# Kernel optimization log

Measured on AMD Instinct MI355X. Metric: run time of the kernel, lower is better.

Reference implementation:

```python
import jax, jax.numpy as jnp
import numpy as np

D_MODEL = 768
NUM_HEADS = 12
SEGMENT_LENGTHS = (2048, 4096, 8192)
DILATION_RATES = (1, 2, 4)
LN_EPS = 1e-5


def setup_inputs() -> dict:
    key = jax.random.key(0)
    ks = jax.random.split(key, 8)
    b, n, dm = 2, 8192, D_MODEL
    s = 1.0 / np.sqrt(dm)
    return {
        "x": jax.random.normal(ks[0], (b, n, dm), dtype=jnp.float32),
        "w_in": jax.random.normal(ks[1], (dm, dm), dtype=jnp.float32) * s,
        "b_in": jnp.zeros((dm,), dtype=jnp.float32),
        "w_out": jax.random.normal(ks[2], (dm, dm), dtype=jnp.float32) * s,
        "b_out": jnp.zeros((dm,), dtype=jnp.float32),
        "ln_gamma": jnp.ones((dm,), dtype=jnp.float32),
        "ln_beta": jnp.zeros((dm,), dtype=jnp.float32),
    }


def _dilated_attention(q, k, v):
    # q, k, v: (b, n, h, d)
    b, n, h, d = q.shape
    num_groups = len(DILATION_RATES)
    group_sizes = [h // num_groups] * num_groups
    for i in range(h % num_groups):
        group_sizes[i] += 1
    scale = 1.0 / jnp.sqrt(jnp.asarray(d, q.dtype))
    out = jnp.zeros_like(q)
    for i, (g, r, s) in enumerate(zip(group_sizes, DILATION_RATES, SEGMENT_LENGTHS)):
        offset = i % r
        hmin, hmax = i * g, (i + 1) * g
        nseg = n // s
        def slc(t):
            # (b, nseg, s, h, d) -> strided dilation slice + head group slice
            return t.reshape(b, nseg, s, h, d)[:, :, offset::r, hmin:hmax, :]
        qs, ks_, vs = slc(q), slc(k), slc(v)  # (b, nseg, se, g, d), se = s // r
        attn = jnp.einsum('bnqhd,bnkhd->bnhqk', qs, ks_) * scale
        attn = jax.nn.softmax(attn, axis=-1)
        x = jnp.einsum('bnhqk,bnkhd->bnqhd', attn, vs)  # (b, nseg, se, g, d)
        # renormalize by sum over (segment, within-segment) dims, as in source
        x = x / x.sum(axis=(1, 2), keepdims=True)
        out = (out.reshape(b, nseg, s, h, d)
                  .at[:, :, offset::r, hmin:hmax, :].add(x)
                  .reshape(b, n, h, d))
    return out / num_groups


def reference(x, w_in, b_in, w_out, b_out, ln_gamma, ln_beta):
    b, n, dm = x.shape
    hd = dm // NUM_HEADS
    # QKVProjectionOption.SAME: q = k = v = proj(x)
    q = x @ w_in.T + b_in
    qh = q.reshape(b, n, NUM_HEADS, hd)
    o = _dilated_attention(qh, qh, qh)
    o = o.reshape(b, n, dm)
    mu = o.mean(axis=-1, keepdims=True)
    var = ((o - mu) ** 2).mean(axis=-1, keepdims=True)
    o = (o - mu) / jnp.sqrt(var + LN_EPS) * ln_gamma + ln_beta
    return o @ w_out.T + b_out
```

## Files before the change

### kernel.cpp

```cpp
#include <hip/hip_runtime.h>
#include <hip/hip_bf16.h>
#include <math.h>

#define B_   2
#define N_   8192
#define DM   768
#define NH   12
#define HD   64

#define QL_ELEM_OFF 12582912ull
#define AC_OFF      12582912ull
#define SUMS_OFF    19922944ull

typedef short bf16x8 __attribute__((ext_vector_type(8)));
typedef _Float16 f16x8 __attribute__((ext_vector_type(8)));
typedef _Float16 f16x4 __attribute__((ext_vector_type(4)));
typedef float f32x4  __attribute__((ext_vector_type(4)));

__device__ __forceinline__ size_t ac_base(int grp) {
    return 8388608ull - (8388608ull >> grp);
}

__device__ __forceinline__ unsigned short f2bf(float f) {
    __hip_bfloat16 h = __float2bfloat16(f);
    return __builtin_bit_cast(unsigned short, h);
}
__device__ __forceinline__ float bf2f(unsigned short u) {
    __hip_bfloat16 h = __builtin_bit_cast(__hip_bfloat16, u);
    return __bfloat162float(h);
}
__device__ __forceinline__ void split2h(float f, _Float16& h, _Float16& l) {
    h = (_Float16)f;
    l = (_Float16)(f - (float)h);
}

#define SW(row, col) ((((row) << 6)) + ((((col) >> 3) ^ ((row) & 7)) << 3) + ((col) & 7))

__global__ __launch_bounds__(256) void gemm_mfma_split(
    const float* __restrict__ A, const float* __restrict__ W,
    const float* __restrict__ bias, float* __restrict__ C,
    _Float16* __restrict__ Ch, _Float16* __restrict__ Cl) {
    __shared__ unsigned short AsH[128][40];
    __shared__ unsigned short AsL[128][40];
    __shared__ unsigned short WsH[128][40];
    __shared__ unsigned short WsL[128][40];

    const int t    = threadIdx.x;
    const int lane = t & 63;
    const int wv   = t >> 6;
    const int c    = lane & 15, q = lane >> 4;
    const int mw   = (wv & 1) * 64, nw = (wv >> 1) * 64;
    const int m0   = blockIdx.x * 128, n0 = blockIdx.y * 128;

    const int srow = t >> 1;
    const int scol = (t & 1) * 16;
    const float* ap = A + (size_t)(m0 + srow) * DM + scol;
    const float* wp = W + (size_t)(n0 + srow) * DM + scol;

    f32x4 acc[4][4];
#pragma unroll
    for (int mi = 0; mi < 4; ++mi)
#pragma unroll
        for (int ni = 0; ni < 4; ++ni) {
            acc[mi][ni][0] = 0.f; acc[mi][ni][1] = 0.f;
            acc[mi][ni][2] = 0.f; acc[mi][ni][3] = 0.f;
        }

    for (int k0 = 0; k0 < DM; k0 += 32) {
        float av[16], wvv[16];
        *(float4*)&av[0]  = *(const float4*)(ap + k0);
        *(float4*)&av[4]  = *(const float4*)(ap + k0 + 4);
        *(float4*)&av[8]  = *(const float4*)(ap + k0 + 8);
        *(float4*)&av[12] = *(const float4*)(ap + k0 + 12);
        *(float4*)&wvv[0]  = *(const float4*)(wp + k0);
        *(float4*)&wvv[4]  = *(const float4*)(wp + k0 + 4);
        *(float4*)&wvv[8]  = *(const float4*)(wp + k0 + 8);
        *(float4*)&wvv[12] = *(const float4*)(wp + k0 + 12);
        __syncthreads();
#pragma unroll
        for (int i = 0; i < 16; ++i) {
            const float x = av[i];
            const unsigned short xh = f2bf(x);
            AsH[srow][scol + i] = xh;
            AsL[srow][scol + i] = f2bf(x - bf2f(xh));
            const float y = wvv[i];
            const unsigned short yh = f2bf(y);
            WsH[srow][scol + i] = yh;
            WsL[srow][scol + i] = f2bf(y - bf2f(yh));
        }
        __syncthreads();

        bf16x8 ah[4], al[4], bh[4], bl[4];
#pragma unroll
        for (int i = 0; i < 4; ++i) {
            ah[i] = *(const bf16x8*)&AsH[mw + i*16 + c][q*8];
            al[i] = *(const bf16x8*)&AsL[mw + i*16 + c][q*8];
            bh[i] = *(const bf16x8*)&WsH[nw + i*16 + c][q*8];
            bl[i] = *(const bf16x8*)&WsL[nw + i*16 + c][q*8];
        }
#pragma unroll
        for (int mi = 0; mi < 4; ++mi)
#pragma unroll
            for (int ni = 0; ni < 4; ++ni) {
                f32x4 v = acc[mi][ni];
                v = __builtin_amdgcn_mfma_f32_16x16x32_bf16(ah[mi], bl[ni], v, 0, 0, 0);
                v = __builtin_amdgcn_mfma_f32_16x16x32_bf16(al[mi], bh[ni], v, 0, 0, 0);
                v = __builtin_amdgcn_mfma_f32_16x16x32_bf16(ah[mi], bh[ni], v, 0, 0, 0);
                acc[mi][ni] = v;
            }
    }

#pragma unroll
    for (int ni = 0; ni < 4; ++ni) {
        const int col = n0 + nw + ni*16 + c;
        const float bv = bias[col];
#pragma unroll
        for (int mi = 0; mi < 4; ++mi)
#pragma unroll
            for (int r = 0; r < 4; ++r) {
                const int row = m0 + mw + mi*16 + q*4 + r;
                const float val = acc[mi][ni][r] + bv;
                if (Ch) {
                    _Float16 hh, ll;
                    split2h(val, hh, ll);
                    Ch[(size_t)row * DM + col] = hh;
                    Cl[(size_t)row * DM + col] = ll;
                } else {
                    C[(size_t)row * DM + col] = val;
                }
            }
    }
}

__global__ __launch_bounds__(256, 2) void attn_mfma_kernel(
    const _Float16* __restrict__ Qh, const _Float16* __restrict__ Ql,
    float* __restrict__ AC) {
    __shared__ __align__(16) _Float16 KH[4096],  KL[4096];
    __shared__ __align__(16) _Float16 VTH[4096], VTL[4096];
    __shared__ __align__(16) _Float16 PTH[8192], PTL[8192];

    const int t    = threadIdx.x;
    const int lane = t & 63;
    const int w    = t >> 6;
    const int c    = lane & 15, quad = lane >> 4;

    const int bi  = blockIdx.x;
    const int qt  = bi & 15;
    const int bsh = bi >> 4;
    int grp, local;
    if (bsh < 32)      { grp = 0; local = bsh; }
    else if (bsh < 48) { grp = 1; local = bsh - 32; }
    else               { grp = 2; local = bsh - 48; }
    const int nseg = 4 >> grp;
    const int sseg = 2048 << grp;
    const int r    = 1 << grp;
    const int b    = local / (nseg * 4);
    const int rem  = local - b * nseg * 4;
    const int seg  = rem >> 2;
    const int hg   = rem & 3;
    const int head = grp * 4 + hg;

    const size_t row0 = (size_t)(b * N_ + seg * sseg + grp);
    const int hoff = head * HD;

    const int r0 = (t >> 4) * 4;
    const int c0 = (t & 15) * 4;

    f16x8 qfh[2][2], qfl[2][2];
#pragma unroll
    for (int jt = 0; jt < 2; ++jt) {
        const int qrow = qt*128 + w*32 + jt*16 + c;
        const size_t qoff = (row0 + (size_t)qrow * r) * DM + hoff;
#pragma unroll
        for (int kc = 0; kc < 2; ++kc) {
            f16x8 h = *(const f16x8*)(Qh + qoff + kc*32 + quad*8);
            f16x8 l = *(const f16x8*)(Ql + qoff + kc*32 + quad*8);
            qfh[jt][kc] = h * (_Float16)0.125f;
            qfl[jt][kc] = l * (_Float16)0.125f;
        }
    }

    {
        f16x4 hh[4], ll[4];
#pragma unroll
        for (int i = 0; i < 4; ++i) {
            const size_t off = (row0 + (size_t)(r0 + i) * r) * DM + hoff + c0;
            hh[i] = *(const f16x4*)(Qh + off);
            ll[i] = *(const f16x4*)(Ql + off);
        }
#pragma unroll
        for (int i = 0; i < 4; ++i) {
            *(f16x4*)&KH[SW(r0 + i, c0)] = hh[i];
            *(f16x4*)&KL[SW(r0 + i, c0)] = ll[i];
        }
#pragma unroll
        for (int j = 0; j < 4; ++j) {
            *(f16x4*)&VTH[SW(c0 + j, r0)] = (f16x4){hh[0][j], hh[1][j], hh[2][j], hh[3][j]};
            *(f16x4*)&VTL[SW(c0 + j, r0)] = (f16x4){ll[0][j], ll[1][j], ll[2][j], ll[3][j]};
        }
    }
    __syncthreads();

    float m_st[2] = {-1e30f, -1e30f};
    float l_st[2] = {0.f, 0.f};
    f32x4 o[2][4];
#pragma unroll
    for (int jt = 0; jt < 2; ++jt)
#pragma unroll
        for (int i = 0; i < 4; ++i) {
            o[jt][i][0] = 0.f; o[jt][i][1] = 0.f;
            o[jt][i][2] = 0.f; o[jt][i][3] = 0.f;
        }

    for (int kt = 0; kt < 32; ++kt) {
        f16x4 nh[4], nl[4];
        if (kt < 31) {
#pragma unroll
            for (int i = 0; i < 4; ++i) {
                const size_t off = (row0 + (size_t)((kt+1)*64 + r0 + i) * r) * DM + hoff + c0;
                nh[i] = *(const f16x4*)(Qh + off);
                nl[i] = *(const f16x4*)(Ql + off);
            }
        }

        f32x4 s[2][4];
#pragma unroll
        for (int jt = 0; jt < 2; ++jt)
#pragma unroll
            for (int mt = 0; mt < 4; ++mt) {
                s[jt][mt][0] = 0.f; s[jt][mt][1] = 0.f;
                s[jt][mt][2] = 0.f; s[jt][mt][3] = 0.f;
            }
#pragma unroll
        for (int kc = 0; kc < 2; ++kc)
#pragma unroll
            for (int mt = 0; mt < 4; ++mt) {
                f16x8 ah = *(const f16x8*)&KH[SW(mt*16 + c, kc*32 + quad*8)];
                f16x8 al = *(const f16x8*)&KL[SW(mt*16 + c, kc*32 + quad*8)];
#pragma unroll
                for (int jt = 0; jt < 2; ++jt) {
                    f32x4 v = s[jt][mt];
                    v = __builtin_amdgcn_mfma_f32_16x16x32_f16(ah, qfl[jt][kc], v, 0, 0, 0);
                    v = __builtin_amdgcn_mfma_f32_16x16x32_f16(al, qfh[jt][kc], v, 0, 0, 0);
                    v = __builtin_amdgcn_mfma_f32_16x16x32_f16(ah, qfh[jt][kc], v, 0, 0, 0);
                    s[jt][mt] = v;
                }
            }

#pragma unroll
        for (int jt = 0; jt < 2; ++jt) {
            float mloc = s[jt][0][0];
#pragma unroll
            for (int mt = 0; mt < 4; ++mt)
#pragma unroll
                for (int rg = 0; rg < 4; ++rg) mloc = fmaxf(mloc, s[jt][mt][rg]);
            mloc = fmaxf(mloc, __shfl_xor(mloc, 16));
            mloc = fmaxf(mloc, __shfl_xor(mloc, 32));
            const float mnew  = fmaxf(m_st[jt], mloc);
            const float alpha = __expf(m_st[jt] - mnew);
            m_st[jt] = mnew;

            float psum = 0.f;
            const int prow = w*32 + jt*16 + c;
#pragma unroll
            for (int mt = 0; mt < 4; ++mt) {
                f16x4 hh, ll;
#pragma unroll
                for (int rg = 0; rg < 4; ++rg) {
                    const float pv = __expf(s[jt][mt][rg] - mnew);
                    psum += pv;
                    _Float16 th, tl;
                    split2h(pv, th, tl);
                    hh[rg] = th;
                    ll[rg] = tl;
                }
                *(f16x4*)&PTH[SW(prow, mt*16 + quad*4)] = hh;
                *(f16x4*)&PTL[SW(prow, mt*16 + quad*4)] = ll;
            }
            psum += __shfl_xor(psum, 16);
            psum += __shfl_xor(psum, 32);
            l_st[jt] = l_st[jt] * alpha + psum;
#pragma unroll
            for (int mtd = 0; mtd < 4; ++mtd) {
                o[jt][mtd][0] *= alpha; o[jt][mtd][1] *= alpha;
                o[jt][mtd][2] *= alpha; o[jt][mtd][3] *= alpha;
            }
        }

#pragma unroll
        for (int kc = 0; kc < 2; ++kc) {
            f16x8 ph[2], pl[2];
#pragma unroll
            for (int jt = 0; jt < 2; ++jt) {
                ph[jt] = *(const f16x8*)&PTH[SW(w*32 + jt*16 + c, kc*32 + quad*8)];
                pl[jt] = *(const f16x8*)&PTL[SW(w*32 + jt*16 + c, kc*32 + quad*8)];
            }
#pragma unroll
            for (int mtd = 0; mtd < 4; ++mtd) {
                f16x8 vh = *(const f16x8*)&VTH[SW(mtd*16 + c, kc*32 + quad*8)];
                f16x8 vl = *(const f16x8*)&VTL[SW(mtd*16 + c, kc*32 + quad*8)];
#pragma unroll
                for (int jt = 0; jt < 2; ++jt) {
                    f32x4 v = o[jt][mtd];
                    v = __builtin_amdgcn_mfma_f32_16x16x32_f16(vh, pl[jt], v, 0, 0, 0);
                    v = __builtin_amdgcn_mfma_f32_16x16x32_f16(vl, ph[jt], v, 0, 0, 0);
                    v = __builtin_amdgcn_mfma_f32_16x16x32_f16(vh, ph[jt], v, 0, 0, 0);
                    o[jt][mtd] = v;
                }
            }
        }

        if (kt < 31) {
            __syncthreads();
#pragma unroll
            for (int i = 0; i < 4; ++i) {
                *(f16x4*)&KH[SW(r0 + i, c0)] = nh[i];
                *(f16x4*)&KL[SW(r0 + i, c0)] = nl[i];
            }
#pragma unroll
            for (int j = 0; j < 4; ++j) {
                *(f16x4*)&VTH[SW(c0 + j, r0)] = (f16x4){nh[0][j], nh[1][j], nh[2][j], nh[3][j]};
                *(f16x4*)&VTL[SW(c0 + j, r0)] = (f16x4){nl[0][j], nl[1][j], nl[2][j], nl[3][j]};
            }
            __syncthreads();
        }
    }

    const size_t gbase = ac_base(grp);
#pragma unroll
    for (int jt = 0; jt < 2; ++jt) {
        const float inv = 1.0f / l_st[jt];
        const int qrow = qt*128 + w*32 + jt*16 + c;
        float* dst = AC + gbase + ((size_t)((b*nseg + seg)*2048 + qrow)) * 256 + hg*64;
#pragma unroll
        for (int mtd = 0; mtd < 4; ++mtd) {
            float4 v = make_float4(o[jt][mtd][0]*inv, o[jt][mtd][1]*inv,
                                   o[jt][mtd][2]*inv, o[jt][mtd][3]*inv);
            *(float4*)(dst + mtd*16 + quad*4) = v;
        }
    }
}

__global__ __launch_bounds__(256) void sum_kernel(
    const float* __restrict__ AC, float* __restrict__ SUMS) {
    const int bi = blockIdx.x;
    int grp, local;
    if (bi < 64)      { grp = 0; local = bi; }
    else if (bi < 96) { grp = 1; local = bi - 64; }
    else              { grp = 2; local = bi - 96; }
    const int chunks = 32 >> grp;
    const int b  = local / chunks;
    const int ch = local - b * chunks;
    const int P  = 8192 >> grp;
    const size_t base = ac_base(grp) + ((size_t)b * P + ch * 256) * 256 + threadIdx.x;
    float acc = 0.f;
    for (int p = 0; p < 256; ++p) acc += AC[base + (size_t)p * 256];
    atomicAdd(&SUMS[((grp << 1) + b) * 256 + threadIdx.x], acc);
}

__device__ __forceinline__ float block_reduce_sum(float val, float* sdata) {
    __syncthreads();
#pragma unroll
    for (int o = 32; o > 0; o >>= 1) val += __shfl_down(val, o);
    const int lane = threadIdx.x & 63, wid = threadIdx.x >> 6;
    if (lane == 0) sdata[wid] = val;
    __syncthreads();
    return sdata[0] + sdata[1] + sdata[2] + sdata[3];
}

__global__ __launch_bounds__(256) void renorm_ln_kernel(
    const float* __restrict__ AC, const float* __restrict__ SUMS,
    const float* __restrict__ gamma, const float* __restrict__ beta,
    float* __restrict__ OLN) {
    __shared__ float sdata[4];
    const int pos = blockIdx.x;
    const int b = pos >> 13;
    const int n = pos & 8191;

    float v[3];
    int dms[3];
#pragma unroll
    for (int jj = 0; jj < 3; ++jj) {
        const int dm = threadIdx.x + (jj << 8);
        dms[jj] = dm;
        const int h = dm >> 6, d = dm & 63;
        const int grp = h >> 2, hg = h & 3;
        const int r = 1 << grp;
        const int p = n & ((2048 << grp) - 1);
        float val = 0.f;
        if ((p & (r - 1)) == grp) {
            const int nseg = 4 >> grp;
            const int seg  = n >> (11 + grp);
            const int j    = (p - grp) >> grp;
            const float s  = SUMS[((grp << 1) + b) * 256 + (hg << 6) + d];
            val = AC[ac_base(grp) + ((size_t)((b*nseg + seg)*2048 + j)) * 256 + (hg << 6) + d]
                  / (3.0f * s);
        }
        v[jj] = val;
    }

    const float tot = block_reduce_sum(v[0] + v[1] + v[2], sdata);
    const float mu  = tot * (1.0f / 768.0f);
    float sq = 0.f;
#pragma unroll
    for (int jj = 0; jj < 3; ++jj) {
        const float d0 = v[jj] - mu;
        sq += d0 * d0;
    }
    const float var  = block_reduce_sum(sq, sdata) * (1.0f / 768.0f);
    const float rstd = rsqrtf(var + 1e-5f);

    float* dst = OLN + (size_t)pos * 768;
#pragma unroll
    for (int jj = 0; jj < 3; ++jj)
        dst[dms[jj]] = (v[jj] - mu) * rstd * gamma[dms[jj]] + beta[dms[jj]];
}

extern "C" void kernel_launch(void* const* d_in, const int* in_sizes, int n_in,
                              void* d_out, int out_size, void* d_ws, size_t ws_size,
                              hipStream_t stream) {
    const float* x     = (const float*)d_in[0];
    const float* w_in  = (const float*)d_in[1];
    const float* b_in  = (const float*)d_in[2];
    const float* w_out = (const float*)d_in[3];
    const float* b_out = (const float*)d_in[4];
    const float* gamma = (const float*)d_in[5];
    const float* beta  = (const float*)d_in[6];
    float* out = (float*)d_out;

    float* ws   = (float*)d_ws;
    _Float16* Qh = (_Float16*)ws;
    _Float16* Ql = (_Float16*)ws + QL_ELEM_OFF;
    float* AC   = ws + AC_OFF;
    float* SUMS = ws + SUMS_OFF;
    float* OLN  = ws;

    gemm_mfma_split<<<dim3(128, 6), 256, 0, stream>>>(x, w_in, b_in, nullptr, Qh, Ql);
    attn_mfma_kernel<<<896, 256, 0, stream>>>(Qh, Ql, AC);
    (void)hipMemsetAsync(SUMS, 0, 1536 * sizeof(float), stream);
    sum_kernel<<<112, 256, 0, stream>>>(AC, SUMS);
    renorm_ln_kernel<<<B_ * N_, 256, 0, stream>>>(AC, SUMS, gamma, beta, OLN);
    gemm_mfma_split<<<dim3(128, 6), 256, 0, stream>>>(OLN, w_out, b_out, out,
                                                      nullptr, nullptr);
}
```

Measured before the change: 571.2 us.

## Halve attention block waves, widen sum grid, use per-wave LayerNorm rows

The attention kernel now runs with 128 threads (2 waves), each wave handling 64 query rows instead of 32. This doubles the MFMA work per K/V LDS fragment load and halves the number of waves competing for LDS, at the cost of more registers per thread and fewer threads for staging K/V. The column-sum kernel is split into 8x more blocks with shorter loops to expose more parallelism. The renorm+LayerNorm kernel maps one wave per row and reduces with shuffles only, removing shared-memory block reductions and __syncthreads.

```diff
diff --git a/kernel.cpp b/kernel.cpp
--- a/kernel.cpp
+++ b/kernel.cpp
@@ -132,7 +132,7 @@
     }
 }
 
-__global__ __launch_bounds__(256, 2) void attn_mfma_kernel(
+__global__ __launch_bounds__(128, 2) void attn_mfma_kernel(
     const _Float16* __restrict__ Qh, const _Float16* __restrict__ Ql,
     float* __restrict__ AC) {
     __shared__ __align__(16) _Float16 KH[4096],  KL[4096];
@@ -163,13 +163,13 @@
     const size_t row0 = (size_t)(b * N_ + seg * sseg + grp);
     const int hoff = head * HD;
 
-    const int r0 = (t >> 4) * 4;
+    const int r0 = (t >> 4) * 8;
     const int c0 = (t & 15) * 4;
 
-    f16x8 qfh[2][2], qfl[2][2];
-#pragma unroll
-    for (int jt = 0; jt < 2; ++jt) {
-        const int qrow = qt*128 + w*32 + jt*16 + c;
+    f16x8 qfh[4][2], qfl[4][2];
+#pragma unroll
+    for (int jt = 0; jt < 4; ++jt) {
+        const int qrow = qt*128 + w*64 + jt*16 + c;
         const size_t qoff = (row0 + (size_t)qrow * r) * DM + hoff;
 #pragma unroll
         for (int kc = 0; kc < 2; ++kc) {
@@ -181,31 +181,33 @@
     }
 
     {
-        f16x4 hh[4], ll[4];
-#pragma unroll
-        for (int i = 0; i < 4; ++i) {
+        f16x4 hh[8], ll[8];
+#pragma unroll
+        for (int i = 0; i < 8; ++i) {
             const size_t off = (row0 + (size_t)(r0 + i) * r) * DM + hoff + c0;
             hh[i] = *(const f16x4*)(Qh + off);
             ll[i] = *(const f16x4*)(Ql + off);
         }
 #pragma unroll
-        for (int i = 0; i < 4; ++i) {
+        for (int i = 0; i < 8; ++i) {
             *(f16x4*)&KH[SW(r0 + i, c0)] = hh[i];
             *(f16x4*)&KL[SW(r0 + i, c0)] = ll[i];
         }
 #pragma unroll
         for (int j = 0; j < 4; ++j) {
-            *(f16x4*)&VTH[SW(c0 + j, r0)] = (f16x4){hh[0][j], hh[1][j], hh[2][j], hh[3][j]};
-            *(f16x4*)&VTL[SW(c0 + j, r0)] = (f16x4){ll[0][j], ll[1][j], ll[2][j], ll[3][j]};
+            *(f16x4*)&VTH[SW(c0 + j, r0)]     = (f16x4){hh[0][j], hh[1][j], hh[2][j], hh[3][j]};
+            *(f16x4*)&VTH[SW(c0 + j, r0 + 4)] = (f16x4){hh[4][j], hh[5][j], hh[6][j], hh[7][j]};
+            *(f16x4*)&VTL[SW(c0 + j, r0)]     = (f16x4){ll[0][j], ll[1][j], ll[2][j], ll[3][j]};
+            *(f16x4*)&VTL[SW(c0 + j, r0 + 4)] = (f16x4){ll[4][j], ll[5][j], ll[6][j], ll[7][j]};
         }
     }
     __syncthreads();
 
-    float m_st[2] = {-1e30f, -1e30f};
-    float l_st[2] = {0.f, 0.f};
-    f32x4 o[2][4];
-#pragma unroll
-    for (int jt = 0; jt < 2; ++jt)
+    float m_st[4] = {-1e30f, -1e30f, -1e30f, -1e30f};
+    float l_st[4] = {0.f, 0.f, 0.f, 0.f};
+    f32x4 o[4][4];
+#pragma unroll
+    for (int jt = 0; jt < 4; ++jt)
 #pragma unroll
         for (int i = 0; i < 4; ++i) {
             o[jt][i][0] = 0.f; o[jt][i][1] = 0.f;
@@ -213,19 +215,19 @@
         }
 
     for (int kt = 0; kt < 32; ++kt) {
-        f16x4 nh[4], nl[4];
+        f16x4 nh[8], nl[8];
         if (kt < 31) {
 #pragma unroll
-            for (int i = 0; i < 4; ++i) {
+            for (int i = 0; i < 8; ++i) {
                 const size_t off = (row0 + (size_t)((kt+1)*64 + r0 + i) * r) * DM + hoff + c0;
                 nh[i] = *(const f16x4*)(Qh + off);
                 nl[i] = *(const f16x4*)(Ql + off);
             }
         }
 
-        f32x4 s[2][4];
-#pragma unroll
-        for (int jt = 0; jt < 2; ++jt)
+        f32x4 s[4][4];
+#pragma unroll
+        for (int jt = 0; jt < 4; ++jt)
 #pragma unroll
             for (int mt = 0; mt < 4; ++mt) {
                 s[jt][mt][0] = 0.f; s[jt][mt][1] = 0.f;
@@ -238,7 +240,7 @@
                 f16x8 ah = *(const f16x8*)&KH[SW(mt*16 + c, kc*32 + quad*8)];
                 f16x8 al = *(const f16x8*)&KL[SW(mt*16 + c, kc*32 + quad*8)];
 #pragma unroll
-                for (int jt = 0; jt < 2; ++jt) {
+                for (int jt = 0; jt < 4; ++jt) {
                     f32x4 v = s[jt][mt];
                     v = __builtin_amdgcn_mfma_f32_16x16x32_f16(ah, qfl[jt][kc], v, 0, 0, 0);
                     v = __builtin_amdgcn_mfma_f32_16x16x32_f16(al, qfh[jt][kc], v, 0, 0, 0);
@@ -248,7 +250,7 @@
             }
 
 #pragma unroll
-        for (int jt = 0; jt < 2; ++jt) {
+        for (int jt = 0; jt < 4; ++jt) {
             float mloc = s[jt][0][0];
 #pragma unroll
             for (int mt = 0; mt < 4; ++mt)
@@ -261,7 +263,7 @@
             m_st[jt] = mnew;
 
             float psum = 0.f;
-            const int prow = w*32 + jt*16 + c;
+            const int prow = w*64 + jt*16 + c;
 #pragma unroll
             for (int mt = 0; mt < 4; ++mt) {
                 f16x4 hh, ll;
@@ -289,18 +291,18 @@
 
 #pragma unroll
         for (int kc = 0; kc < 2; ++kc) {
-            f16x8 ph[2], pl[2];
-#pragma unroll
-            for (int jt = 0; jt < 2; ++jt) {
-                ph[jt] = *(const f16x8*)&PTH[SW(w*32 + jt*16 + c, kc*32 + quad*8)];
-                pl[jt] = *(const f16x8*)&PTL[SW(w*32 + jt*16 + c, kc*32 + quad*8)];
+            f16x8 ph[4], pl[4];
+#pragma unroll
+            for (int jt = 0; jt < 4; ++jt) {
+                ph[jt] = *(const f16x8*)&PTH[SW(w*64 + jt*16 + c, kc*32 + quad*8)];
+                pl[jt] = *(const f16x8*)&PTL[SW(w*64 + jt*16 + c, kc*32 + quad*8)];
             }
 #pragma unroll
             for (int mtd = 0; mtd < 4; ++mtd) {
                 f16x8 vh = *(const f16x8*)&VTH[SW(mtd*16 + c, kc*32 + quad*8)];
                 f16x8 vl = *(const f16x8*)&VTL[SW(mtd*16 + c, kc*32 + quad*8)];
 #pragma unroll
-                for (int jt = 0; jt < 2; ++jt) {
+                for (int jt = 0; jt < 4; ++jt) {
                     f32x4 v = o[jt][mtd];
                     v = __builtin_amdgcn_mfma_f32_16x16x32_f16(vh, pl[jt], v, 0, 0, 0);
                     v = __builtin_amdgcn_mfma_f32_16x16x32_f16(vl, ph[jt], v, 0, 0, 0);
@@ -313,14 +315,16 @@
         if (kt < 31) {
             __syncthreads();
 #pragma unroll
-            for (int i = 0; i < 4; ++i) {
+            for (int i = 0; i < 8; ++i) {
                 *(f16x4*)&KH[SW(r0 + i, c0)] = nh[i];
                 *(f16x4*)&KL[SW(r0 + i, c0)] = nl[i];
             }
 #pragma unroll
             for (int j = 0; j < 4; ++j) {
-                *(f16x4*)&VTH[SW(c0 + j, r0)] = (f16x4){nh[0][j], nh[1][j], nh[2][j], nh[3][j]};
-                *(f16x4*)&VTL[SW(c0 + j, r0)] = (f16x4){nl[0][j], nl[1][j], nl[2][j], nl[3][j]};
+                *(f16x4*)&VTH[SW(c0 + j, r0)]     = (f16x4){nh[0][j], nh[1][j], nh[2][j], nh[3][j]};
+                *(f16x4*)&VTH[SW(c0 + j, r0 + 4)] = (f16x4){nh[4][j], nh[5][j], nh[6][j], nh[7][j]};
+                *(f16x4*)&VTL[SW(c0 + j, r0)]     = (f16x4){nl[0][j], nl[1][j], nl[2][j], nl[3][j]};
+                *(f16x4*)&VTL[SW(c0 + j, r0 + 4)] = (f16x4){nl[4][j], nl[5][j], nl[6][j], nl[7][j]};
             }
             __syncthreads();
         }
@@ -328,9 +332,9 @@
 
     const size_t gbase = ac_base(grp);
 #pragma unroll
-    for (int jt = 0; jt < 2; ++jt) {
+    for (int jt = 0; jt < 4; ++jt) {
         const float inv = 1.0f / l_st[jt];
-        const int qrow = qt*128 + w*32 + jt*16 + c;
+        const int qrow = qt*128 + w*64 + jt*16 + c;
         float* dst = AC + gbase + ((size_t)((b*nseg + seg)*2048 + qrow)) * 256 + hg*64;
 #pragma unroll
         for (int mtd = 0; mtd < 4; ++mtd) {
@@ -345,46 +349,32 @@
     const float* __restrict__ AC, float* __restrict__ SUMS) {
     const int bi = blockIdx.x;
     int grp, local;
-    if (bi < 64)      { grp = 0; local = bi; }
-    else if (bi < 96) { grp = 1; local = bi - 64; }
-    else              { grp = 2; local = bi - 96; }
-    const int chunks = 32 >> grp;
+    if (bi < 512)      { grp = 0; local = bi; }
+    else if (bi < 768) { grp = 1; local = bi - 512; }
+    else               { grp = 2; local = bi - 768; }
+    const int chunks = 256 >> grp;
     const int b  = local / chunks;
     const int ch = local - b * chunks;
     const int P  = 8192 >> grp;
-    const size_t base = ac_base(grp) + ((size_t)b * P + ch * 256) * 256 + threadIdx.x;
+    const size_t base = ac_base(grp) + ((size_t)b * P + ch * 32) * 256 + threadIdx.x;
     float acc = 0.f;
-    for (int p = 0; p < 256; ++p) acc += AC[base + (size_t)p * 256];
+    for (int p = 0; p < 32; ++p) acc += AC[base + (size_t)p * 256];
     atomicAdd(&SUMS[((grp << 1) + b) * 256 + threadIdx.x], acc);
-}
-
-__device__ __forceinline__ float block_reduce_sum(float val, float* sdata) {
-    __syncthreads();
-#pragma unroll
-    for (int o = 32; o > 0; o >>= 1) val += __shfl_down(val, o);
-    const int lane = threadIdx.x & 63, wid = threadIdx.x >> 6;
-    if (lane == 0) sdata[wid] = val;
-    __syncthreads();
-    return sdata[0] + sdata[1] + sdata[2] + sdata[3];
 }
 
 __global__ __launch_bounds__(256) void renorm_ln_kernel(
     const float* __restrict__ AC, const float* __restrict__ SUMS,
     const float* __restrict__ gamma, const float* __restrict__ beta,
     float* __restrict__ OLN) {
-    __shared__ float sdata[4];
-    const int pos = blockIdx.x;
+    const int pos = blockIdx.x * 4 + (threadIdx.x >> 6);
+    const int l   = threadIdx.x & 63;
     const int b = pos >> 13;
     const int n = pos & 8191;
 
-    float v[3];
-    int dms[3];
-#pragma unroll
-    for (int jj = 0; jj < 3; ++jj) {
-        const int dm = threadIdx.x + (jj << 8);
-        dms[jj] = dm;
-        const int h = dm >> 6, d = dm & 63;
-        const int grp = h >> 2, hg = h & 3;
+    float v[12];
+#pragma unroll
+    for (int jj = 0; jj < 12; ++jj) {
+        const int grp = jj >> 2, hg = jj & 3;
         const int r = 1 << grp;
         const int p = n & ((2048 << grp) - 1);
         float val = 0.f;
@@ -392,28 +382,36 @@
             const int nseg = 4 >> grp;
             const int seg  = n >> (11 + grp);
             const int j    = (p - grp) >> grp;
-            const float s  = SUMS[((grp << 1) + b) * 256 + (hg << 6) + d];
-            val = AC[ac_base(grp) + ((size_t)((b*nseg + seg)*2048 + j)) * 256 + (hg << 6) + d]
+            const float s  = SUMS[((grp << 1) + b) * 256 + (hg << 6) + l];
+            val = AC[ac_base(grp) + ((size_t)((b*nseg + seg)*2048 + j)) * 256 + (hg << 6) + l]
                   / (3.0f * s);
         }
         v[jj] = val;
     }
 
-    const float tot = block_reduce_sum(v[0] + v[1] + v[2], sdata);
-    const float mu  = tot * (1.0f / 768.0f);
+    float tot = 0.f;
+#pragma unroll
+    for (int jj = 0; jj < 12; ++jj) tot += v[jj];
+#pragma unroll
+    for (int o = 32; o > 0; o >>= 1) tot += __shfl_xor(tot, o);
+    const float mu = tot * (1.0f / 768.0f);
+
     float sq = 0.f;
 #pragma unroll
-    for (int jj = 0; jj < 3; ++jj) {
+    for (int jj = 0; jj < 12; ++jj) {
         const float d0 = v[jj] - mu;
         sq += d0 * d0;
     }
-    const float var  = block_reduce_sum(sq, sdata) * (1.0f / 768.0f);
-    const float rstd = rsqrtf(var + 1e-5f);
+#pragma unroll
+    for (int o = 32; o > 0; o >>= 1) sq += __shfl_xor(sq, o);
+    const float rstd = rsqrtf(sq * (1.0f / 768.0f) + 1e-5f);
 
     float* dst = OLN + (size_t)pos * 768;
 #pragma unroll
-    for (int jj = 0; jj < 3; ++jj)
-        dst[dms[jj]] = (v[jj] - mu) * rstd * gamma[dms[jj]] + beta[dms[jj]];
+    for (int jj = 0; jj < 12; ++jj) {
+        const int dm = jj*64 + l;
+        dst[dm] = (v[jj] - mu) * rstd * gamma[dm] + beta[dm];
+    }
 }
 
 extern "C" void kernel_launch(void* const* d_in, const int* in_sizes, int n_in,
@@ -436,10 +434,10 @@
     float* OLN  = ws;
 
     gemm_mfma_split<<<dim3(128, 6), 256, 0, stream>>>(x, w_in, b_in, nullptr, Qh, Ql);
-    attn_mfma_kernel<<<896, 256, 0, stream>>>(Qh, Ql, AC);
+    attn_mfma_kernel<<<896, 128, 0, stream>>>(Qh, Ql, AC);
     (void)hipMemsetAsync(SUMS, 0, 1536 * sizeof(float), stream);
-    sum_kernel<<<112, 256, 0, stream>>>(AC, SUMS);
-    renorm_ln_kernel<<<B_ * N_, 256, 0, stream>>>(AC, SUMS, gamma, beta, OLN);
+    sum_kernel<<<896, 256, 0, stream>>>(AC, SUMS);
+    renorm_ln_kernel<<<B_ * N_ / 4, 256, 0, stream>>>(AC, SUMS, gamma, beta, OLN);
     gemm_mfma_split<<<dim3(128, 6), 256, 0, stream>>>(OLN, w_out, b_out, out,
                                                       nullptr, nullptr);
 }
```

Result: slower. 619.5 us (+8.4%).
